# Optimization experiments

Measured on AMD Instinct MI355X. Metric: run time of the kernel, lower is better.

## Reference

```python
import jax, jax.numpy as jnp
import numpy as np

B, S, D, H = 4, 2048, 1024, 16
HD = D // H  # head_dim = 64


def setup_inputs() -> dict:
    key = jax.random.key(0)
    ks = jax.random.split(key, 8)
    scale = 1.0 / np.sqrt(D)
    return {
        "hidden_states": jax.random.normal(ks[0], (B, S, D), dtype=jnp.float32),
        "attention_mask": jnp.zeros((B, 1, 1, S), dtype=jnp.float32),
        "Wq": jax.random.normal(ks[1], (D, D), dtype=jnp.float32) * scale,
        "bq": jnp.zeros((D,), dtype=jnp.float32),
        "Wk": jax.random.normal(ks[2], (D, D), dtype=jnp.float32) * scale,
        "bk": jnp.zeros((D,), dtype=jnp.float32),
        "Wv": jax.random.normal(ks[3], (D, D), dtype=jnp.float32) * scale,
        "bv": jnp.zeros((D,), dtype=jnp.float32),
    }


def reference(hidden_states, attention_mask, Wq, bq, Wk, bk, Wv, bv):
    def split_heads(x):
        # [B,S,D] -> [B,H,S,HD]
        return x.reshape(B, S, H, HD).transpose(0, 2, 1, 3)

    q = split_heads(hidden_states @ Wq + bq)
    k = split_heads(hidden_states @ Wk + bk)
    v = split_heads(hidden_states @ Wv + bv)

    # [B,H,S,S]
    scores = jnp.einsum("bhqd,bhkd->bhqk", q, k) / jnp.sqrt(jnp.float32(HD))
    scores = scores + attention_mask  # additive mask, broadcasts [B,1,1,S]
    probs = jax.nn.softmax(scores, axis=-1)

    ctx = jnp.einsum("bhqk,bhkd->bhqd", probs, v)  # [B,H,S,HD]
    return ctx.transpose(0, 2, 1, 3).reshape(B, S, D)
```

## Files before the change

kernel.cpp:

```cpp
#include <hip/hip_runtime.h>
#include <hip/hip_bf16.h>
#include <stdint.h>

typedef __attribute__((ext_vector_type(4))) float f32x4;
typedef __attribute__((ext_vector_type(16))) float f32x16;
typedef __attribute__((ext_vector_type(8))) short bf16x8;
typedef __attribute__((ext_vector_type(4))) int int4v;
typedef __attribute__((ext_vector_type(8))) unsigned short u16x8;
typedef unsigned int u32;

static __device__ __forceinline__ unsigned short f2bf(float f) {
    union { float f; unsigned u; } v; v.f = f;
    unsigned r = v.u + 0x7FFF + ((v.u >> 16) & 1);
    return (unsigned short)(r >> 16);
}

static __device__ __forceinline__ u32 cvtpk(float lo, float hi) {
    u32 r;
    asm("v_cvt_pk_bf16_f32 %0, %1, %2" : "=v"(r) : "v"(lo), "v"(hi));
    return r;
}

__global__ __launch_bounds__(256) void cvt_x_kernel(const float* __restrict__ x,
                                                    unsigned short* __restrict__ xb) {
    int i = (blockIdx.x * 256 + threadIdx.x) * 4;
    float4 v = *(const float4*)(x + i);
    ushort4 o = make_ushort4(f2bf(v.x), f2bf(v.y), f2bf(v.z), f2bf(v.w));
    *(ushort4*)(xb + i) = o;
}

__global__ __launch_bounds__(256) void cvt_w_kernel(const float* __restrict__ Wq,
                                                    const float* __restrict__ Wk,
                                                    const float* __restrict__ Wv,
                                                    unsigned short* __restrict__ Wt3) {
    const float* W = (blockIdx.z == 0) ? Wq : ((blockIdx.z == 1) ? Wk : Wv);
    unsigned short* out = Wt3 + (size_t)blockIdx.z * 1024 * 1024;
    __shared__ unsigned short t[64][68];
    int k0 = blockIdx.x * 64, n0 = blockIdx.y * 64;
    int tid = threadIdx.x;
#pragma unroll
    for (int i = 0; i < 4; i++) {
        int c = i * 256 + tid;
        int row = c >> 4, cb = c & 15;
        float4 v = *(const float4*)(W + (size_t)(k0 + row) * 1024 + n0 + cb * 4);
        ushort4 o = make_ushort4(f2bf(v.x), f2bf(v.y), f2bf(v.z), f2bf(v.w));
        *(ushort4*)(&t[row][cb * 4]) = o;
    }
    __syncthreads();
#pragma unroll
    for (int i = 0; i < 2; i++) {
        int c = i * 256 + tid;
        int n = c >> 3, kc = c & 7;
        u16x8 tmp;
#pragma unroll
        for (int j = 0; j < 8; j++) tmp[j] = t[kc * 8 + j][n];
        *(u16x8*)(&out[(size_t)(n0 + n) * 1024 + k0 + kc * 8]) = tmp;
    }
}

__global__ __launch_bounds__(256) void mask_reorder_kernel(const float* __restrict__ mask,
                                                           float* __restrict__ maskr) {
    int o = blockIdx.x * 256 + threadIdx.x;
    int reg = o & 15, kvb = (o >> 4) & 1, hi2 = (o >> 5) & 1, kt = (o >> 6) & 31, bb = o >> 11;
    int kv = kt * 64 + kvb * 32 + (reg & 3) + 8 * (reg >> 2) + 4 * hi2;
    maskr[o] = 8.0f * mask[bb * 2048 + kv];
}

__global__ __launch_bounds__(256) void qkv_gemm_kernel(
    const unsigned short* __restrict__ Xb,
    const unsigned short* __restrict__ Wt3,
    const float* __restrict__ bq, const float* __restrict__ bk, const float* __restrict__ bv,
    unsigned short* __restrict__ Qo, unsigned short* __restrict__ Ko,
    unsigned short* __restrict__ Vt)
{
    int z = blockIdx.z;
    const unsigned short* Wt = Wt3 + (size_t)z * 1048576;
    const float* bias = (z == 0) ? bq : ((z == 1) ? bk : bv);
    int m0 = blockIdx.x * 128, n0 = blockIdx.y * 128;

    __shared__ unsigned short As[128 * 64];
    __shared__ unsigned short Bs[128 * 64];

    int tid = threadIdx.x, lane = tid & 63, wave = tid >> 6;
    int wm = wave >> 1, wn = wave & 1;
    int lr = lane & 15, lg = lane >> 4;
    int swzf = (lr & 7) << 4;

    f32x4 acc[4][4] = {};

    for (int kt = 0; kt < 16; kt++) {
        int kbase = kt * 64;
#pragma unroll
        for (int i = 0; i < 4; i++) {
            int c = i * 256 + tid;
            int row = c >> 3, cb = c & 7;
            int4v av = *(const int4v*)(Xb + (size_t)(m0 + row) * 1024 + kbase + cb * 8);
            int4v bv2 = *(const int4v*)(Wt + (size_t)(n0 + row) * 1024 + kbase + cb * 8);
            int off = row * 128 + ((cb * 16) ^ ((row & 7) << 4));
            *(int4v*)((char*)As + off) = av;
            *(int4v*)((char*)Bs + off) = bv2;
        }
        __syncthreads();
#pragma unroll
        for (int kk = 0; kk < 2; kk++) {
            bf16x8 a[4], bb[4];
#pragma unroll
            for (int mi = 0; mi < 4; mi++)
                a[mi] = *(const bf16x8*)((char*)As + (wm * 64 + mi * 16 + lr) * 128
                                         + ((kk * 64 + lg * 16) ^ swzf));
#pragma unroll
            for (int ni = 0; ni < 4; ni++)
                bb[ni] = *(const bf16x8*)((char*)Bs + (wn * 64 + ni * 16 + lr) * 128
                                          + ((kk * 64 + lg * 16) ^ swzf));
#pragma unroll
            for (int mi = 0; mi < 4; mi++)
#pragma unroll
                for (int ni = 0; ni < 4; ni++)
                    acc[mi][ni] = __builtin_amdgcn_mfma_f32_16x16x32_bf16(a[mi], bb[ni], acc[mi][ni], 0, 0, 0);
        }
        __syncthreads();
    }

    if (z < 2) {
        unsigned short* out = (z == 0) ? Qo : Ko;
#pragma unroll
        for (int ni = 0; ni < 4; ni++) {
            int n = n0 + wn * 64 + ni * 16 + lr;
            float bsv = bias[n];
#pragma unroll
            for (int mi = 0; mi < 4; mi++) {
                int mrow = m0 + wm * 64 + mi * 16 + lg * 4;
#pragma unroll
                for (int r = 0; r < 4; r++)
                    out[(size_t)(mrow + r) * 1024 + n] = f2bf(acc[mi][ni][r] + bsv);
            }
        }
    } else {
#pragma unroll
        for (int ni = 0; ni < 4; ni++) {
            int n = n0 + wn * 64 + ni * 16 + lr;
            float bsv = bias[n];
            int h = n >> 6, hd = n & 63;
#pragma unroll
            for (int mi = 0; mi < 4; mi++) {
                int mrow = m0 + wm * 64 + mi * 16 + lg * 4;
                int b = mrow >> 11, s = mrow & 2047;
                ushort4 pk = make_ushort4(f2bf(acc[mi][ni][0] + bsv),
                                          f2bf(acc[mi][ni][1] + bsv),
                                          f2bf(acc[mi][ni][2] + bsv),
                                          f2bf(acc[mi][ni][3] + bsv));
                *(ushort4*)(&Vt[((size_t)(b * 16 + h) * 64 + hd) * 2048 + s]) = pk;
            }
        }
    }
}

__global__ __launch_bounds__(256) void attn_kernel(
    const unsigned short* __restrict__ Q,
    const unsigned short* __restrict__ K,
    const unsigned short* __restrict__ Vt,
    const float* __restrict__ maskr,
    float* __restrict__ out)
{
    __shared__ __align__(16) char smem[16640];
    const int tid = threadIdx.x, lane = tid & 63, w = tid >> 6;
    const int ln31 = lane & 31, hi = lane >> 5;
    const int bh = blockIdx.y, b = bh >> 4, h = bh & 15;
    const int q0 = blockIdx.x * 128 + w * 32;
    const int swz = (ln31 & 7) << 4;
    const float c1 = 0.18033688011112042f;

    const unsigned short* Qrow = Q + (size_t)(b * 2048 + q0 + ln31) * 1024 + h * 64;
    bf16x8 aq[4];
#pragma unroll
    for (int ds = 0; ds < 4; ds++) aq[ds] = *(const bf16x8*)(Qrow + ds * 16 + hi * 8);

    const unsigned short* Kbp = K + (size_t)b * 2048 * 1024 + h * 64;
    const unsigned short* Vbp = Vt + (size_t)bh * 64 * 2048;
    const float* mbase = maskr + (size_t)b * 2048;

    const int r0 = tid >> 3, cb = tid & 7;
    const int woff = (cb * 16) ^ ((r0 & 7) << 4);
    char* KsW0 = smem + r0 * 128 + woff;
    char* KsW1 = smem + (r0 + 32) * 128 + woff;
    char* VsW0 = KsW0 + 8192;
    char* VsW1 = KsW1 + 8192;

    f32x16 oacc0 = {}, oacc1 = {};
    float mrun = -1e30f, lrun = 0.f;

    int4v kr0, kr1, vr0, vr1, mr = {};
    {
        const size_t ko = (size_t)r0 * 1024 + cb * 8;
        kr0 = *(const int4v*)(Kbp + ko);
        kr1 = *(const int4v*)(Kbp + 32 * 1024 + ko);
        vr0 = *(const int4v*)(Vbp + (size_t)r0 * 2048 + cb * 8);
        vr1 = *(const int4v*)(Vbp + (size_t)(r0 + 32) * 2048 + cb * 8);
        if (tid < 16) mr = *(const int4v*)(mbase + tid * 4);
    }

    char* KsL = smem + ln31 * 128;
    char* VsL = smem + 8192 + ln31 * 128;
    const f32x4* mpl = (const f32x4*)(smem + 16384) + hi * 8;

    for (int kt = 0; kt < 32; kt++) {
        __syncthreads();
        *(int4v*)KsW0 = kr0; *(int4v*)KsW1 = kr1;
        *(int4v*)VsW0 = vr0; *(int4v*)VsW1 = vr1;
        if (tid < 16) *(int4v*)(smem + 16384 + tid * 16) = mr;
        __syncthreads();
        if (kt < 31) {
            const int kv0 = (kt + 1) * 64;
            const size_t ko = (size_t)(kv0 + r0) * 1024 + cb * 8;
            kr0 = *(const int4v*)(Kbp + ko);
            kr1 = *(const int4v*)(Kbp + 32 * 1024 + ko);
            vr0 = *(const int4v*)(Vbp + (size_t)r0 * 2048 + kv0 + cb * 8);
            vr1 = *(const int4v*)(Vbp + (size_t)(r0 + 32) * 2048 + kv0 + cb * 8);
            if (tid < 16) mr = *(const int4v*)(mbase + (kv0) + tid * 4);
        }

        f32x16 st0, st1;
        {
            f32x4 m0 = mpl[0], m1 = mpl[1], m2 = mpl[2], m3 = mpl[3];
            f32x4 m4 = mpl[4], m5 = mpl[5], m6 = mpl[6], m7 = mpl[7];
#pragma unroll
            for (int j = 0; j < 4; j++) {
                st0[j] = m0[j]; st0[4 + j] = m1[j]; st0[8 + j] = m2[j]; st0[12 + j] = m3[j];
                st1[j] = m4[j]; st1[4 + j] = m5[j]; st1[8 + j] = m6[j]; st1[12 + j] = m7[j];
            }
        }
#pragma unroll
        for (int ds = 0; ds < 4; ds++) {
            const int co = (ds * 32 + hi * 16) ^ swz;
            bf16x8 ka0 = *(const bf16x8*)(KsL + co);
            bf16x8 ka1 = *(const bf16x8*)(KsL + 4096 + co);
            st0 = __builtin_amdgcn_mfma_f32_32x32x16_bf16(ka0, aq[ds], st0, 0, 0, 0);
            st1 = __builtin_amdgcn_mfma_f32_32x32x16_bf16(ka1, aq[ds], st1, 0, 0, 0);
        }

        float mx = st0[0];
#pragma unroll
        for (int j = 1; j < 16; j++) mx = fmaxf(mx, st0[j]);
#pragma unroll
        for (int j = 0; j < 16; j++) mx = fmaxf(mx, st1[j]);
        mx = fmaxf(mx, __shfl_xor(mx, 32));
        const float mnew = fmaxf(mrun, mx);
        const float alpha = __builtin_amdgcn_exp2f((mrun - mnew) * c1);
        mrun = mnew;
        const float mc = mnew * c1;
        float sum = 0.f;
#pragma unroll
        for (int j = 0; j < 16; j++) { float v = __builtin_amdgcn_exp2f(st0[j] * c1 - mc); st0[j] = v; sum += v; }
#pragma unroll
        for (int j = 0; j < 16; j++) { float v = __builtin_amdgcn_exp2f(st1[j] * c1 - mc); st1[j] = v; sum += v; }
        sum += __shfl_xor(sum, 32);
        lrun = lrun * alpha + sum;
#pragma unroll
        for (int j = 0; j < 16; j++) { oacc0[j] *= alpha; oacc1[j] *= alpha; }

#pragma unroll
        for (int s = 0; s < 4; s++) {
            const f32x16& pp = (s & 2) ? st1 : st0;
            const int rA = (s & 1) * 8, rB = rA + 4;
            u32 cl0 = cvtpk(pp[rA + 0], pp[rA + 1]);
            u32 cl1 = cvtpk(pp[rA + 2], pp[rA + 3]);
            u32 ch0 = cvtpk(pp[rB + 0], pp[rB + 1]);
            u32 ch1 = cvtpk(pp[rB + 2], pp[rB + 3]);
            u32 sl0 = __shfl_xor(cl0, 32), sl1 = __shfl_xor(cl1, 32);
            u32 sh0 = __shfl_xor(ch0, 32), sh1 = __shfl_xor(ch1, 32);
            union { u32 u[4]; bf16x8 v; } pb;
            pb.u[0] = hi ? sh0 : cl0;
            pb.u[1] = hi ? sh1 : cl1;
            pb.u[2] = hi ? ch0 : sl0;
            pb.u[3] = hi ? ch1 : sl1;
            const int co = (s * 32 + hi * 16) ^ swz;
            bf16x8 va0 = *(const bf16x8*)(VsL + co);
            bf16x8 va1 = *(const bf16x8*)(VsL + 4096 + co);
            oacc0 = __builtin_amdgcn_mfma_f32_32x32x16_bf16(va0, pb.v, oacc0, 0, 0, 0);
            oacc1 = __builtin_amdgcn_mfma_f32_32x32x16_bf16(va1, pb.v, oacc1, 0, 0, 0);
        }
    }

    __syncthreads();
    const float rl = 1.0f / lrun;
    float* lw = (float*)(smem + w * 4096);
    const int qp = lane >> 1, hb = (lane & 1) * 16;
#pragma unroll
    for (int p = 0; p < 2; p++) {
        const f32x16& oa = p ? oacc1 : oacc0;
#pragma unroll
        for (int r = 0; r < 16; r++) {
            int hd = (r & 3) + 8 * (r >> 2) + 4 * hi;
            lw[hd * 32 + ln31] = oa[r] * rl;
        }
        float* od = out + (size_t)(b * 2048 + q0 + qp) * 1024 + h * 64 + p * 32 + hb;
#pragma unroll
        for (int c = 0; c < 4; c++) {
            f32x4 o4;
#pragma unroll
            for (int j = 0; j < 4; j++) o4[j] = lw[(hb + c * 4 + j) * 32 + qp];
            *(f32x4*)(od + c * 4) = o4;
        }
    }
}

extern "C" void kernel_launch(void* const* d_in, const int* in_sizes, int n_in,
                              void* d_out, int out_size, void* d_ws, size_t ws_size,
                              hipStream_t stream) {
    const float* hs   = (const float*)d_in[0];
    const float* mask = (const float*)d_in[1];
    const float* Wq   = (const float*)d_in[2];
    const float* bq   = (const float*)d_in[3];
    const float* Wk   = (const float*)d_in[4];
    const float* bk   = (const float*)d_in[5];
    const float* Wv   = (const float*)d_in[6];
    const float* bv   = (const float*)d_in[7];
    float* out = (float*)d_out;

    char* ws = (char*)d_ws;
    unsigned short* Xb  = (unsigned short*)ws;
    unsigned short* Wt3 = (unsigned short*)(ws + 16777216);
    unsigned short* Qb  = (unsigned short*)(ws + 16777216 + 6291456);
    unsigned short* Kb  = Qb + 8388608;
    unsigned short* Vt  = Kb + 8388608;
    float* maskr = (float*)(ws + 16777216 + 6291456 + 3 * 16777216);

    cvt_x_kernel<<<8192, 256, 0, stream>>>(hs, Xb);
    cvt_w_kernel<<<dim3(16, 16, 3), 256, 0, stream>>>(Wq, Wk, Wv, Wt3);
    mask_reorder_kernel<<<32, 256, 0, stream>>>(mask, maskr);
    qkv_gemm_kernel<<<dim3(64, 8, 3), 256, 0, stream>>>(Xb, Wt3, bq, bk, bv, Qb, Kb, Vt);
    attn_kernel<<<dim3(16, 64), 256, 0, stream>>>(Qb, Kb, Vt, maskr, out);
}
```

Before: 220.8 us.

## Double-buffer K/V LDS tiles, lazy softmax rescale, permlane swap in attention

The attention kernel now double-buffers K, V and mask tiles in LDS, so each iteration needs one barrier instead of two, and global loads are issued two tiles ahead. The online-softmax rescale is skipped unless the row max grows past a threshold, max and sum reductions use trees, and the P repacking uses v_permlane32_swap instead of four shuffles. It also raises wave priority around the MFMA blocks. In exchange LDS use doubles, which can lower occupancy, and the lazy rescale relies on a fixed exponent headroom, which risks overflow if scores vary widely.

```diff
diff --git a/kernel.cpp b/kernel.cpp
--- a/kernel.cpp
+++ b/kernel.cpp
@@ -19,6 +19,10 @@
     u32 r;
     asm("v_cvt_pk_bf16_f32 %0, %1, %2" : "=v"(r) : "v"(lo), "v"(hi));
     return r;
+}
+
+static __device__ __forceinline__ void pl32swap_u(u32& a, u32& b) {
+    asm("v_permlane32_swap_b32 %0, %1" : "+v"(a), "+v"(b));
 }
 
 __global__ __launch_bounds__(256) void cvt_x_kernel(const float* __restrict__ x,
@@ -162,13 +166,14 @@
     const float* __restrict__ maskr,
     float* __restrict__ out)
 {
-    __shared__ __align__(16) char smem[16640];
+    __shared__ __align__(16) char smem[33280];
     const int tid = threadIdx.x, lane = tid & 63, w = tid >> 6;
     const int ln31 = lane & 31, hi = lane >> 5;
     const int bh = blockIdx.y, b = bh >> 4, h = bh & 15;
     const int q0 = blockIdx.x * 128 + w * 32;
     const int swz = (ln31 & 7) << 4;
     const float c1 = 0.18033688011112042f;
+    const float DTHR = 44.361f;
 
     const unsigned short* Qrow = Q + (size_t)(b * 2048 + q0 + ln31) * 1024 + h * 64;
     bf16x8 aq[4];
@@ -177,58 +182,52 @@
 
     const unsigned short* Kbp = K + (size_t)b * 2048 * 1024 + h * 64;
     const unsigned short* Vbp = Vt + (size_t)bh * 64 * 2048;
-    const float* mbase = maskr + (size_t)b * 2048;
 
     const int r0 = tid >> 3, cb = tid & 7;
-    const int woff = (cb * 16) ^ ((r0 & 7) << 4);
-    char* KsW0 = smem + r0 * 128 + woff;
-    char* KsW1 = smem + (r0 + 32) * 128 + woff;
-    char* VsW0 = KsW0 + 8192;
-    char* VsW1 = KsW1 + 8192;
+    const int woff = r0 * 128 + ((cb * 16) ^ ((r0 & 7) << 4));
+
+    const unsigned short* kp = Kbp + (size_t)r0 * 1024 + cb * 8;
+    const unsigned short* vp = Vbp + (size_t)r0 * 2048 + cb * 8;
+    const float* mp = maskr + (size_t)b * 2048 + tid * 4;
 
     f32x16 oacc0 = {}, oacc1 = {};
     float mrun = -1e30f, lrun = 0.f;
 
     int4v kr0, kr1, vr0, vr1, mr = {};
-    {
-        const size_t ko = (size_t)r0 * 1024 + cb * 8;
-        kr0 = *(const int4v*)(Kbp + ko);
-        kr1 = *(const int4v*)(Kbp + 32 * 1024 + ko);
-        vr0 = *(const int4v*)(Vbp + (size_t)r0 * 2048 + cb * 8);
-        vr1 = *(const int4v*)(Vbp + (size_t)(r0 + 32) * 2048 + cb * 8);
-        if (tid < 16) mr = *(const int4v*)(mbase + tid * 4);
-    }
-
-    char* KsL = smem + ln31 * 128;
-    char* VsL = smem + 8192 + ln31 * 128;
-    const f32x4* mpl = (const f32x4*)(smem + 16384) + hi * 8;
-
+    kr0 = *(const int4v*)kp; kr1 = *(const int4v*)(kp + 32 * 1024);
+    vr0 = *(const int4v*)vp; vr1 = *(const int4v*)(vp + 32 * 2048);
+    if (tid < 16) mr = *(const int4v*)mp;
+    kp += 65536; vp += 64; mp += 64;
+    *(int4v*)(smem + woff) = kr0;
+    *(int4v*)(smem + 32 * 128 + woff) = kr1;
+    *(int4v*)(smem + 16384 + woff) = vr0;
+    *(int4v*)(smem + 16384 + 32 * 128 + woff) = vr1;
+    if (tid < 16) *(int4v*)(smem + 32768 + tid * 16) = mr;
+    kr0 = *(const int4v*)kp; kr1 = *(const int4v*)(kp + 32 * 1024);
+    vr0 = *(const int4v*)vp; vr1 = *(const int4v*)(vp + 32 * 2048);
+    if (tid < 16) mr = *(const int4v*)mp;
+    kp += 65536; vp += 64; mp += 64;
+    __syncthreads();
+
+#pragma unroll 2
     for (int kt = 0; kt < 32; kt++) {
-        __syncthreads();
-        *(int4v*)KsW0 = kr0; *(int4v*)KsW1 = kr1;
-        *(int4v*)VsW0 = vr0; *(int4v*)VsW1 = vr1;
-        if (tid < 16) *(int4v*)(smem + 16384 + tid * 16) = mr;
-        __syncthreads();
-        if (kt < 31) {
-            const int kv0 = (kt + 1) * 64;
-            const size_t ko = (size_t)(kv0 + r0) * 1024 + cb * 8;
-            kr0 = *(const int4v*)(Kbp + ko);
-            kr1 = *(const int4v*)(Kbp + 32 * 1024 + ko);
-            vr0 = *(const int4v*)(Vbp + (size_t)r0 * 2048 + kv0 + cb * 8);
-            vr1 = *(const int4v*)(Vbp + (size_t)(r0 + 32) * 2048 + kv0 + cb * 8);
-            if (tid < 16) mr = *(const int4v*)(mbase + (kv0) + tid * 4);
-        }
+        const int cur = kt & 1;
+        const char* KsL = smem + cur * 8192 + ln31 * 128;
+        const char* VsL = KsL + 16384;
+        const f32x4* mpl = (const f32x4*)(smem + 32768 + cur * 256 + hi * 128);
 
         f32x16 st0, st1;
         {
-            f32x4 m0 = mpl[0], m1 = mpl[1], m2 = mpl[2], m3 = mpl[3];
-            f32x4 m4 = mpl[4], m5 = mpl[5], m6 = mpl[6], m7 = mpl[7];
+            f32x4 a0 = mpl[0], a1 = mpl[1], a2 = mpl[2], a3 = mpl[3];
+            f32x4 a4 = mpl[4], a5 = mpl[5], a6 = mpl[6], a7 = mpl[7];
 #pragma unroll
             for (int j = 0; j < 4; j++) {
-                st0[j] = m0[j]; st0[4 + j] = m1[j]; st0[8 + j] = m2[j]; st0[12 + j] = m3[j];
-                st1[j] = m4[j]; st1[4 + j] = m5[j]; st1[8 + j] = m6[j]; st1[12 + j] = m7[j];
+                st0[j] = a0[j]; st0[4 + j] = a1[j]; st0[8 + j] = a2[j]; st0[12 + j] = a3[j];
+                st1[j] = a4[j]; st1[4 + j] = a5[j]; st1[8 + j] = a6[j]; st1[12 + j] = a7[j];
             }
         }
+
+        __builtin_amdgcn_s_setprio(1);
 #pragma unroll
         for (int ds = 0; ds < 4; ds++) {
             const int co = (ds * 32 + hi * 16) ^ swz;
@@ -237,51 +236,80 @@
             st0 = __builtin_amdgcn_mfma_f32_32x32x16_bf16(ka0, aq[ds], st0, 0, 0, 0);
             st1 = __builtin_amdgcn_mfma_f32_32x32x16_bf16(ka1, aq[ds], st1, 0, 0, 0);
         }
-
-        float mx = st0[0];
-#pragma unroll
-        for (int j = 1; j < 16; j++) mx = fmaxf(mx, st0[j]);
-#pragma unroll
-        for (int j = 0; j < 16; j++) mx = fmaxf(mx, st1[j]);
+        __builtin_amdgcn_s_setprio(0);
+
+        float t16[16];
+#pragma unroll
+        for (int j = 0; j < 16; j++) t16[j] = fmaxf(st0[j], st1[j]);
+#pragma unroll
+        for (int stp = 8; stp > 0; stp >>= 1)
+#pragma unroll
+            for (int j = 0; j < 8; j++) if (j < stp) t16[j] = fmaxf(t16[j], t16[j + stp]);
+        float mx = t16[0];
         mx = fmaxf(mx, __shfl_xor(mx, 32));
-        const float mnew = fmaxf(mrun, mx);
-        const float alpha = __builtin_amdgcn_exp2f((mrun - mnew) * c1);
-        mrun = mnew;
-        const float mc = mnew * c1;
-        float sum = 0.f;
-#pragma unroll
-        for (int j = 0; j < 16; j++) { float v = __builtin_amdgcn_exp2f(st0[j] * c1 - mc); st0[j] = v; sum += v; }
-#pragma unroll
-        for (int j = 0; j < 16; j++) { float v = __builtin_amdgcn_exp2f(st1[j] * c1 - mc); st1[j] = v; sum += v; }
+
+        if (__any(mx > mrun + DTHR)) {
+            const float mnew = fmaxf(mrun, mx);
+            const float al = __builtin_amdgcn_exp2f((mrun - mnew) * c1);
+            mrun = mnew;
+            lrun *= al;
+#pragma unroll
+            for (int j = 0; j < 16; j++) { oacc0[j] *= al; oacc1[j] *= al; }
+        }
+        const float mc = mrun * c1;
+        float s16[16];
+#pragma unroll
+        for (int j = 0; j < 16; j++) {
+            float v0 = __builtin_amdgcn_exp2f(__builtin_fmaf(st0[j], c1, -mc));
+            float v1 = __builtin_amdgcn_exp2f(__builtin_fmaf(st1[j], c1, -mc));
+            st0[j] = v0; st1[j] = v1; s16[j] = v0 + v1;
+        }
+#pragma unroll
+        for (int stp = 8; stp > 0; stp >>= 1)
+#pragma unroll
+            for (int j = 0; j < 8; j++) if (j < stp) s16[j] += s16[j + stp];
+        float sum = s16[0];
         sum += __shfl_xor(sum, 32);
-        lrun = lrun * alpha + sum;
-#pragma unroll
-        for (int j = 0; j < 16; j++) { oacc0[j] *= alpha; oacc1[j] *= alpha; }
-
+        lrun += sum;
+
+        __builtin_amdgcn_s_setprio(1);
 #pragma unroll
         for (int s = 0; s < 4; s++) {
             const f32x16& pp = (s & 2) ? st1 : st0;
             const int rA = (s & 1) * 8, rB = rA + 4;
-            u32 cl0 = cvtpk(pp[rA + 0], pp[rA + 1]);
-            u32 cl1 = cvtpk(pp[rA + 2], pp[rA + 3]);
-            u32 ch0 = cvtpk(pp[rB + 0], pp[rB + 1]);
-            u32 ch1 = cvtpk(pp[rB + 2], pp[rB + 3]);
-            u32 sl0 = __shfl_xor(cl0, 32), sl1 = __shfl_xor(cl1, 32);
-            u32 sh0 = __shfl_xor(ch0, 32), sh1 = __shfl_xor(ch1, 32);
+            u32 w0 = cvtpk(pp[rA + 0], pp[rA + 1]);
+            u32 w1 = cvtpk(pp[rA + 2], pp[rA + 3]);
+            u32 w2 = cvtpk(pp[rB + 0], pp[rB + 1]);
+            u32 w3 = cvtpk(pp[rB + 2], pp[rB + 3]);
+            pl32swap_u(w0, w2);
+            pl32swap_u(w1, w3);
             union { u32 u[4]; bf16x8 v; } pb;
-            pb.u[0] = hi ? sh0 : cl0;
-            pb.u[1] = hi ? sh1 : cl1;
-            pb.u[2] = hi ? ch0 : sl0;
-            pb.u[3] = hi ? ch1 : sl1;
+            pb.u[0] = w0; pb.u[1] = w1; pb.u[2] = w2; pb.u[3] = w3;
             const int co = (s * 32 + hi * 16) ^ swz;
             bf16x8 va0 = *(const bf16x8*)(VsL + co);
             bf16x8 va1 = *(const bf16x8*)(VsL + 4096 + co);
             oacc0 = __builtin_amdgcn_mfma_f32_32x32x16_bf16(va0, pb.v, oacc0, 0, 0, 0);
             oacc1 = __builtin_amdgcn_mfma_f32_32x32x16_bf16(va1, pb.v, oacc1, 0, 0, 0);
         }
-    }
-
-    __syncthreads();
+        __builtin_amdgcn_s_setprio(0);
+
+        if (kt < 31) {
+            char* base = smem + (cur ^ 1) * 8192;
+            *(int4v*)(base + woff) = kr0;
+            *(int4v*)(base + 32 * 128 + woff) = kr1;
+            *(int4v*)(base + 16384 + woff) = vr0;
+            *(int4v*)(base + 16384 + 32 * 128 + woff) = vr1;
+            if (tid < 16) *(int4v*)(smem + 32768 + (cur ^ 1) * 256 + tid * 16) = mr;
+            if (kt < 30) {
+                kr0 = *(const int4v*)kp; kr1 = *(const int4v*)(kp + 32 * 1024);
+                vr0 = *(const int4v*)vp; vr1 = *(const int4v*)(vp + 32 * 2048);
+                if (tid < 16) mr = *(const int4v*)mp;
+                kp += 65536; vp += 64; mp += 64;
+            }
+        }
+        __syncthreads();
+    }
+
     const float rl = 1.0f / lrun;
     float* lw = (float*)(smem + w * 4096);
     const int qp = lane >> 1, hb = (lane & 1) * 16;
@@ -301,6 +329,7 @@
             for (int j = 0; j < 4; j++) o4[j] = lw[(hb + c * 4 + j) * 32 + qp];
             *(f32x4*)(od + c * 4) = o4;
         }
+        __syncthreads();
     }
 }
 
```

Result: faster. 195.9 us (-11.3%).
